# Optimization experiments

Hardware: AMD Instinct MI355X
Metric: run time of the kernel (lower is better)

The kernel has to match this reference:

```python
import jax, jax.numpy as jnp
import numpy as np

N_NODES = 100000
N_EDGES = 1000000
IN_CH = 64
HID = 64
PROJ = 128
N_GRAPHS = 64
BN_EPS = 1e-5


def _glorot(key, shape):
    fan_in, fan_out = shape[0], shape[1]
    lim = (6.0 / (fan_in + fan_out)) ** 0.5
    return jax.random.uniform(key, shape, jnp.float32, -lim, lim)


def setup_inputs() -> dict:
    key = jax.random.key(0)
    ks = jax.random.split(key, 16)
    x = jax.random.normal(ks[0], (N_NODES, IN_CH), jnp.float32)
    edge_index = jax.random.randint(ks[1], (2, N_EDGES), 0, N_NODES, jnp.int64)
    batch = jnp.sort(jax.random.randint(ks[2], (N_NODES,), 0, N_GRAPHS, jnp.int64))
    inp = {
        "x": x, "edge_index": edge_index, "batch": batch,
        # conv1 MLP: Linear(2*in, hid), Linear(hid, hid)
        "c1_w1": _glorot(ks[3], (2 * IN_CH, HID)), "c1_b1": jnp.zeros((HID,), jnp.float32),
        "c1_w2": _glorot(ks[4], (HID, HID)), "c1_b2": jnp.zeros((HID,), jnp.float32),
        "bn1_g": jnp.ones((HID,), jnp.float32), "bn1_b": jnp.zeros((HID,), jnp.float32),
        # conv2 MLP: Linear(2*hid, hid), Linear(hid, hid)
        "c2_w1": _glorot(ks[5], (2 * HID, HID)), "c2_b1": jnp.zeros((HID,), jnp.float32),
        "c2_w2": _glorot(ks[6], (HID, HID)), "c2_b2": jnp.zeros((HID,), jnp.float32),
        "bn2_g": jnp.ones((HID,), jnp.float32), "bn2_b": jnp.zeros((HID,), jnp.float32),
        # projector: Linear(2*hid, proj), BN(proj), Linear(proj, proj)
        "p_w1": _glorot(ks[7], (2 * HID, PROJ)), "p_b1": jnp.zeros((PROJ,), jnp.float32),
        "p_bng": jnp.ones((PROJ,), jnp.float32), "p_bnb": jnp.zeros((PROJ,), jnp.float32),
        "p_w2": _glorot(ks[8], (PROJ, PROJ)), "p_b2": jnp.zeros((PROJ,), jnp.float32),
    }
    return inp


def _edge_conv(x, src, dst, w1, b1, w2, b2):
    # PyG EdgeConv: message = nn(cat([x_i, x_j - x_i])), aggr = max over incoming edges
    xi = x[dst]                                   # [E, C] target features
    xj = x[src]                                   # [E, C] source features
    m = jnp.concatenate([xi, xj - xi], axis=-1)   # [E, 2C]
    h = jax.nn.relu(m @ w1 + b1)
    h = jax.nn.relu(h @ w2 + b2)                  # [E, H]
    out = jax.ops.segment_max(h, dst, num_segments=N_NODES)
    return jnp.where(jnp.isfinite(out), out, 0.0)  # nodes w/o in-edges -> 0


def _batchnorm(x, g, b):
    mu = jnp.mean(x, axis=0)
    var = jnp.mean((x - mu) ** 2, axis=0)  # biased var (training-mode BN)
    return (x - mu) * jax.lax.rsqrt(var + BN_EPS) * g + b


def reference(x, edge_index, batch,
              c1_w1, c1_b1, c1_w2, c1_b2, bn1_g, bn1_b,
              c2_w1, c2_b1, c2_w2, c2_b2, bn2_g, bn2_b,
              p_w1, p_b1, p_bng, p_bnb, p_w2, p_b2):
    src, dst = edge_index[0], edge_index[1]
    h = _edge_conv(x, src, dst, c1_w1, c1_b1, c1_w2, c1_b2)
    h = _batchnorm(h, bn1_g, bn1_b)
    h = _edge_conv(h, src, dst, c2_w1, c2_b1, c2_w2, c2_b2)
    x_node = _batchnorm(h, bn2_g, bn2_b)            # [N, H]
    # graph pooling
    counts = jax.ops.segment_sum(jnp.ones((N_NODES,), x_node.dtype), batch,
                                 num_segments=N_GRAPHS)
    mean_pool = jax.ops.segment_sum(x_node, batch, num_segments=N_GRAPHS) / \
        jnp.maximum(counts, 1.0)[:, None]
    max_pool = jax.ops.segment_max(x_node, batch, num_segments=N_GRAPHS)
    max_pool = jnp.where(jnp.isfinite(max_pool), max_pool, 0.0)
    x_graph = jnp.concatenate([mean_pool, max_pool], axis=1)  # [G, 2H]
    # projector MLP
    z = x_graph @ p_w1 + p_b1
    z = jax.nn.relu(_batchnorm(z, p_bng, p_bnb))
    z_proj = z @ p_w2 + p_b2                        # [G, PROJ]
    return (z_proj, x_node, x_graph)
```

## Files before the change

### kernel.cpp

```cpp
#include <hip/hip_runtime.h>
#include <hip/hip_fp16.h>

constexpr int NN = 100000;
constexpr int NE = 1000000;
constexpr int NG = 64;
constexpr float BN_EPS = 1e-5f;
constexpr int NTILES = NE / 32;
constexpr int NNTILES = NN / 32;
constexpr int NREC = NTILES * 2;

constexpr int NBUK = 196;
constexpr int BINB = 256;
constexpr int BCHUNK = (NE + BINB - 1) / BINB;
constexpr int TABN = NBUK * BINB;

constexpr long H1R_OFF  = 0;
constexpr long XNR_OFF  = 3200000;
constexpr long PART_OFF = 6400000;
constexpr long SC1_OFF  = PART_OFF + 32768;
constexpr long SH1_OFF  = SC1_OFF + 64;
constexpr long SC2_OFF  = SH1_OFF + 64;
constexpr long SH2_OFF  = SC2_OFF + 64;
constexpr long PSUM_OFF = SH2_OFF + 64;
constexpr long PMAX_OFF = PSUM_OFF + 4096;
constexpr long CNT_OFF  = PMAX_OFF + 4096;
constexpr long TAB_OFF  = CNT_OFF + 64;
constexpr long SEDG_OFF = TAB_OFF + 50176;
constexpr long WF1_OFF  = SEDG_OFF + 2000000;
constexpr long WF2_OFF  = WF1_OFF + 6144;
constexpr long RECD_OFF = WF2_OFF + 6144;
constexpr long RECV_OFF = RECD_OFF + 62528;
constexpr long P_OFF    = RECV_OFF + 2000000;
constexpr long Q_OFF    = P_OFF + 3200000;

constexpr long OUT_XNODE = 8192;
constexpr long OUT_XG    = 8192 + 6400000L;

using f16x8 = __attribute__((ext_vector_type(8))) _Float16;
using f32x16 = __attribute__((ext_vector_type(16))) float;

__device__ __forceinline__ unsigned short f2h(float f) {
    return __builtin_bit_cast(unsigned short, (_Float16)f);
}
__device__ __forceinline__ unsigned pkrtz(float a, float b) {
    return __builtin_bit_cast(unsigned, __builtin_amdgcn_cvt_pkrtz(a, b));
}
__device__ __forceinline__ unsigned pk_add_f16(unsigned a, unsigned b) {
    unsigned d;
    asm("v_pk_add_f16 %0, %1, %2" : "=v"(d) : "v"(a), "v"(b));
    return d;
}
__device__ __forceinline__ unsigned pk_max_f16(unsigned a, unsigned b) {
    unsigned d;
    asm("v_pk_max_f16 %0, %1, %2" : "=v"(d) : "v"(a), "v"(b));
    return d;
}
__device__ __forceinline__ float h2f_lo(unsigned u) {
    return (float)__builtin_bit_cast(_Float16, (unsigned short)(u & 0xffffu));
}
__device__ __forceinline__ float h2f_hi(unsigned u) {
    return (float)__builtin_bit_cast(_Float16, (unsigned short)(u >> 16));
}
__device__ __forceinline__ unsigned fenc(float f) {
    unsigned u = __float_as_uint(f);
    return (u & 0x80000000u) ? ~u : (u | 0x80000000u);
}
__device__ __forceinline__ float fdec(unsigned u) {
    return (u & 0x80000000u) ? __uint_as_float(u & 0x7fffffffu) : __uint_as_float(~u);
}
__device__ __forceinline__ int xcd_swz(int bid, int nwg) {
    const int q = nwg >> 3, r = nwg & 7;
    const int x = bid & 7, i = bid >> 3;
    return (x < r ? x * (q + 1) : r * (q + 1) + (x - r) * q) + i;
}

__global__ __launch_bounds__(256) void bin_hist_kernel(
    const int* __restrict__ dst, int* __restrict__ tab)
{
    __shared__ int cnt[NBUK];
    const int t = threadIdx.x, b = blockIdx.x;
    if (t < NBUK) cnt[t] = 0;
    __syncthreads();
    const int lo = b * BCHUNK;
    const int hi = (lo + BCHUNK < NE) ? lo + BCHUNK : NE;
    for (int e = lo + t; e < hi; e += 256) atomicAdd(&cnt[dst[e] >> 9], 1);
    __syncthreads();
    if (t < NBUK) tab[t * BINB + b] = cnt[t];
}

__global__ __launch_bounds__(1024) void scan_tab_kernel(int* __restrict__ tab)
{
    __shared__ int part[1024];
    const int t = threadIdx.x;
    constexpr int VPT = 49;
    int vals[VPT];
    const int base = t * VPT;
    int s = 0;
    #pragma unroll
    for (int i = 0; i < VPT; ++i) {
        const int idx = base + i;
        const int v = (idx < TABN) ? tab[idx] : 0;
        vals[i] = v; s += v;
    }
    part[t] = s;
    __syncthreads();
    for (int off = 1; off < 1024; off <<= 1) {
        const int u = (t >= off) ? part[t - off] : 0;
        __syncthreads();
        part[t] += u;
        __syncthreads();
    }
    int run = (t == 0) ? 0 : part[t - 1];
    #pragma unroll
    for (int i = 0; i < VPT; ++i) {
        const int idx = base + i;
        if (idx < TABN) { const int v = vals[i]; tab[idx] = run; run += v; }
    }
}

__global__ __launch_bounds__(256) void bin_scatter_kernel(
    const int* __restrict__ src, const int* __restrict__ dst,
    const int* __restrict__ tab, int2* __restrict__ ebin)
{
    __shared__ int basec[NBUK];
    __shared__ int cur[NBUK];
    const int t = threadIdx.x, b = blockIdx.x;
    if (t < NBUK) { basec[t] = tab[t * BINB + b]; cur[t] = 0; }
    __syncthreads();
    const int lo = b * BCHUNK;
    const int hi = (lo + BCHUNK < NE) ? lo + BCHUNK : NE;
    for (int e = lo + t; e < hi; e += 256) {
        const int d = dst[e];
        const int k = d >> 9;
        const int pos = basec[k] + atomicAdd(&cur[k], 1);
        ebin[pos] = make_int2(src[e], d);
    }
}

__global__ __launch_bounds__(256) void bucket_sort_kernel(
    const int2* __restrict__ ebin, const int* __restrict__ tab,
    int2* __restrict__ sedge)
{
    __shared__ int hist[512];
    __shared__ int part[256];
    const int t = threadIdx.x, k = blockIdx.x;
    const int start = tab[k * BINB];
    const int end = (k == NBUK - 1) ? NE : tab[(k + 1) * BINB];
    hist[t * 2] = 0; hist[t * 2 + 1] = 0;
    __syncthreads();
    for (int e = start + t; e < end; e += 256) atomicAdd(&hist[ebin[e].y & 511], 1);
    __syncthreads();
    const int v0 = hist[t * 2], v1 = hist[t * 2 + 1];
    part[t] = v0 + v1;
    __syncthreads();
    for (int off = 1; off < 256; off <<= 1) {
        const int u = (t >= off) ? part[t - off] : 0;
        __syncthreads();
        part[t] += u;
        __syncthreads();
    }
    int run = (t == 0) ? 0 : part[t - 1];
    hist[t * 2] = run;
    hist[t * 2 + 1] = run + v0;
    __syncthreads();
    for (int e = start + t; e < end; e += 256) {
        const int2 v = ebin[e];
        const int pos = start + atomicAdd(&hist[v.y & 511], 1);
        sedge[pos] = v;
    }
}

__global__ __launch_bounds__(256) void prep_weights(
    const float* __restrict__ w1, const float* __restrict__ w2,
    unsigned short* __restrict__ wf)
{
    const int idx = blockIdx.x * 256 + threadIdx.x;
    if (idx >= 12288) return;
    const int sec = idx >> 12;
    const int j = idx & 4095;
    const int f = j >> 9, rem = j & 511, ln = rem >> 3, i = rem & 7;
    const int t = f >> 2, ks = f & 3;
    const int k = ks * 16 + (ln >> 5) * 8 + i, c = t * 32 + (ln & 31);
    float v;
    if (sec == 0)      v = w1[k * 64 + c] - w1[(64 + k) * 64 + c];
    else if (sec == 1) v = w1[(64 + k) * 64 + c];
    else               v = w2[k * 64 + c];
    wf[idx] = f2h(v);
}

template<bool NORM>
__global__ __launch_bounds__(256) void nodegemm_kernel(
    const void* __restrict__ xin,
    const unsigned short* __restrict__ wfrag,
    const float* __restrict__ b1,
    const float* __restrict__ scale, const float* __restrict__ shift,
    unsigned short* __restrict__ P, unsigned short* __restrict__ Q)
{
    __shared__ unsigned short wlds[8192];
    {
        const uint4* wsrc = reinterpret_cast<const uint4*>(wfrag);
        uint4* wdst = reinterpret_cast<uint4*>(wlds);
        #pragma unroll
        for (int i = 0; i < 4; ++i) wdst[threadIdx.x + i * 256] = wsrc[threadIdx.x + i * 256];
    }
    __syncthreads();

    const int wid = threadIdx.x >> 6, lane = threadIdx.x & 63;
    const int hi = lane >> 5, ln32 = lane & 31;
    const int tile = blockIdx.x * 4 + wid;
    if (tile >= NNTILES) return;
    const int node = tile * 32 + ln32;

    f32x16 cpa, cpb, cqa, cqb;
    #pragma unroll
    for (int r = 0; r < 16; ++r) {
        const int row = (r & 3) + 8 * (r >> 2) + 4 * hi;
        cpa[r] = b1[row]; cpb[r] = b1[32 + row];
        cqa[r] = 0.f;     cqb[r] = 0.f;
    }

    #pragma unroll
    for (int ks = 0; ks < 4; ++ks) {
        const int off = ks * 16 + hi * 8;
        float4 a, b;
        if constexpr (!NORM) {
            const float* xr = reinterpret_cast<const float*>(xin) + (long)node * 64;
            a = *reinterpret_cast<const float4*>(xr + off);
            b = *reinterpret_cast<const float4*>(xr + off + 4);
        } else {
            const unsigned* xr = reinterpret_cast<const unsigned*>(xin) + (long)node * 32;
            const uint4 u = *reinterpret_cast<const uint4*>(xr + ks * 8 + hi * 4);
            a.x = h2f_lo(u.x); a.y = h2f_hi(u.x); a.z = h2f_lo(u.y); a.w = h2f_hi(u.y);
            b.x = h2f_lo(u.z); b.y = h2f_hi(u.z); b.z = h2f_lo(u.w); b.w = h2f_hi(u.w);
            const float4 s0 = *reinterpret_cast<const float4*>(scale + off);
            const float4 s1 = *reinterpret_cast<const float4*>(scale + off + 4);
            const float4 h0 = *reinterpret_cast<const float4*>(shift + off);
            const float4 h1 = *reinterpret_cast<const float4*>(shift + off + 4);
            a.x = fmaf(a.x, s0.x, h0.x); a.y = fmaf(a.y, s0.y, h0.y);
            a.z = fmaf(a.z, s0.z, h0.z); a.w = fmaf(a.w, s0.w, h0.w);
            b.x = fmaf(b.x, s1.x, h1.x); b.y = fmaf(b.y, s1.y, h1.y);
            b.z = fmaf(b.z, s1.z, h1.z); b.w = fmaf(b.w, s1.w, h1.w);
        }
        uint4 uu;
        uu.x = pkrtz(a.x, a.y); uu.y = pkrtz(a.z, a.w);
        uu.z = pkrtz(b.x, b.y); uu.w = pkrtz(b.z, b.w);
        const f16x8 bfr = __builtin_bit_cast(f16x8, uu);
        const f16x8 ap0 = *reinterpret_cast<const f16x8*>(&wlds[(0 * 4 + ks) * 512 + lane * 8]);
        const f16x8 ap1 = *reinterpret_cast<const f16x8*>(&wlds[(1 * 4 + ks) * 512 + lane * 8]);
        const f16x8 aq0 = *reinterpret_cast<const f16x8*>(&wlds[4096 + (0 * 4 + ks) * 512 + lane * 8]);
        const f16x8 aq1 = *reinterpret_cast<const f16x8*>(&wlds[4096 + (1 * 4 + ks) * 512 + lane * 8]);
        cpa = __builtin_amdgcn_mfma_f32_32x32x16_f16(ap0, bfr, cpa, 0, 0, 0);
        cpb = __builtin_amdgcn_mfma_f32_32x32x16_f16(ap1, bfr, cpb, 0, 0, 0);
        cqa = __builtin_amdgcn_mfma_f32_32x32x16_f16(aq0, bfr, cqa, 0, 0, 0);
        cqb = __builtin_amdgcn_mfma_f32_32x32x16_f16(aq1, bfr, cqb, 0, 0, 0);
    }

    unsigned short* Pr = P + (long)node * 64;
    unsigned short* Qr = Q + (long)node * 64;
    #pragma unroll
    for (int t = 0; t < 2; ++t) {
        const f32x16 cp = t ? cpb : cpa;
        const f32x16 cq = t ? cqb : cqa;
        #pragma unroll
        for (int g2 = 0; g2 < 4; ++g2) {
            uint2 up, uq;
            up.x = pkrtz(cp[4 * g2 + 0], cp[4 * g2 + 1]);
            up.y = pkrtz(cp[4 * g2 + 2], cp[4 * g2 + 3]);
            uq.x = pkrtz(cq[4 * g2 + 0], cq[4 * g2 + 1]);
            uq.y = pkrtz(cq[4 * g2 + 2], cq[4 * g2 + 3]);
            const int co = t * 32 + 8 * g2 + 4 * hi;
            *reinterpret_cast<uint2*>(Pr + co) = up;
            *reinterpret_cast<uint2*>(Qr + co) = uq;
        }
    }
}

__global__ __launch_bounds__(256) void edgeconv_kernel(
    const unsigned short* __restrict__ P, const unsigned short* __restrict__ Q,
    const int2* __restrict__ sedge,
    const unsigned short* __restrict__ w2frag,
    const float* __restrict__ b2,
    unsigned* __restrict__ out,
    int* __restrict__ recd, unsigned* __restrict__ recv)
{
    __shared__ unsigned short wlds[4096];
    {
        const uint4* wsrc = reinterpret_cast<const uint4*>(w2frag);
        uint4* wdst = reinterpret_cast<uint4*>(wlds);
        #pragma unroll
        for (int i = 0; i < 2; ++i) wdst[threadIdx.x + i * 256] = wsrc[threadIdx.x + i * 256];
    }
    __syncthreads();

    const int wid  = threadIdx.x >> 6;
    const int lane = threadIdx.x & 63;
    const int hi   = lane >> 5;
    const int ln32 = lane & 31;
    const int tile = xcd_swz(blockIdx.x, gridDim.x) * 4 + wid;
    if (tile >= NTILES) return;

    const int2 sd = sedge[tile * 32 + ln32];
    const int s = sd.x, d = sd.y;
    const unsigned short* __restrict__ Pr = P + (long)d * 64;
    const unsigned short* __restrict__ Qr = Q + (long)s * 64;

    f32x16 c2a, c2b;
    #pragma unroll
    for (int r = 0; r < 16; ++r) {
        const int row = (r & 3) + 8 * (r >> 2) + 4 * hi;
        c2a[r] = b2[row];
        c2b[r] = b2[32 + row];
    }

    #pragma unroll
    for (int ks = 0; ks < 4; ++ks) {
        const int co = ks * 16 + hi * 8;
        const uint4 pu = *reinterpret_cast<const uint4*>(Pr + co);
        const uint4 qu = *reinterpret_cast<const uint4*>(Qr + co);
        uint4 hh;
        hh.x = pk_max_f16(pk_add_f16(pu.x, qu.x), 0u);
        hh.y = pk_max_f16(pk_add_f16(pu.y, qu.y), 0u);
        hh.z = pk_max_f16(pk_add_f16(pu.z, qu.z), 0u);
        hh.w = pk_max_f16(pk_add_f16(pu.w, qu.w), 0u);
        const f16x8 bfr = __builtin_bit_cast(f16x8, hh);
        const f16x8 a0 = *reinterpret_cast<const f16x8*>(&wlds[(0 * 4 + ks) * 512 + lane * 8]);
        const f16x8 a1 = *reinterpret_cast<const f16x8*>(&wlds[(1 * 4 + ks) * 512 + lane * 8]);
        c2a = __builtin_amdgcn_mfma_f32_32x32x16_f16(a0, bfr, c2a, 0, 0, 0);
        c2b = __builtin_amdgcn_mfma_f32_32x32x16_f16(a1, bfr, c2b, 0, 0, 0);
    }

    unsigned pkc[16];
    #pragma unroll
    for (int q = 0; q < 8; ++q) {
        pkc[q]     = pk_max_f16(pkrtz(c2a[2 * q], c2a[2 * q + 1]), 0u);
        pkc[8 + q] = pk_max_f16(pkrtz(c2b[2 * q], c2b[2 * q + 1]), 0u);
    }

    #pragma unroll
    for (int st = 1; st < 32; st <<= 1) {
        const int dn = __shfl_down(d, st, 32);
        const bool take = (ln32 + st < 32) && (dn == d);
        #pragma unroll
        for (int i = 0; i < 16; ++i) {
            const unsigned o = __shfl_down(pkc[i], st, 32);
            const unsigned m = pk_max_f16(pkc[i], o);
            pkc[i] = take ? m : pkc[i];
        }
    }
    const int dprev = __shfl_up(d, 1, 32);
    const bool leader = (ln32 == 0) || (d != dprev);
    const unsigned lm = (unsigned)(__ballot(leader) & 0xffffffffull);
    const int L31 = 31 - __builtin_clz(lm);

    if (leader) {
        if (ln32 != 0 && ln32 != L31) {
            unsigned* row = out + (long)d * 32;
            #pragma unroll
            for (int g2 = 0; g2 < 4; ++g2) {
                *reinterpret_cast<uint2*>(row + 4 * g2 + 2 * hi) =
                    make_uint2(pkc[2 * g2], pkc[2 * g2 + 1]);
                *reinterpret_cast<uint2*>(row + 16 + 4 * g2 + 2 * hi) =
                    make_uint2(pkc[8 + 2 * g2], pkc[8 + 2 * g2 + 1]);
            }
        }
        if (ln32 == 0) {
            unsigned* row = recv + (long)(tile * 2) * 32;
            #pragma unroll
            for (int g2 = 0; g2 < 4; ++g2) {
                *reinterpret_cast<uint2*>(row + 4 * g2 + 2 * hi) =
                    make_uint2(pkc[2 * g2], pkc[2 * g2 + 1]);
                *reinterpret_cast<uint2*>(row + 16 + 4 * g2 + 2 * hi) =
                    make_uint2(pkc[8 + 2 * g2], pkc[8 + 2 * g2 + 1]);
            }
            if (hi == 0) recd[tile * 2] = d;
        }
        if (ln32 == L31) {
            unsigned* row = recv + (long)(tile * 2 + 1) * 32;
            #pragma unroll
            for (int g2 = 0; g2 < 4; ++g2) {
                *reinterpret_cast<uint2*>(row + 4 * g2 + 2 * hi) =
                    make_uint2(pkc[2 * g2], pkc[2 * g2 + 1]);
                *reinterpret_cast<uint2*>(row + 16 + 4 * g2 + 2 * hi) =
                    make_uint2(pkc[8 + 2 * g2], pkc[8 + 2 * g2 + 1]);
            }
            if (hi == 0) recd[tile * 2 + 1] = d;
        }
    }
}

__global__ __launch_bounds__(256) void fixup_kernel(
    const int* __restrict__ recd, const unsigned* __restrict__ recv,
    unsigned* __restrict__ out)
{
    const int wid = threadIdx.x >> 6;
    const int half = (threadIdx.x >> 5) & 1;
    const int c2 = threadIdx.x & 31;
    const int r = blockIdx.x * 8 + wid * 2 + half;
    if (r >= NREC) return;
    const int d = recd[r];
    int lo = r, hi = r;
    while (lo > 0 && recd[lo - 1] == d) --lo;
    while (hi + 1 < NREC && recd[hi + 1] == d) ++hi;
    unsigned m = 0u;
    for (int rr = lo; rr <= hi; ++rr) m = pk_max_f16(m, recv[(long)rr * 32 + c2]);
    out[(long)d * 32 + c2] = m;
}

__global__ __launch_bounds__(256) void stats_kernel(
    const unsigned* __restrict__ h, float* __restrict__ partial)
{
    __shared__ float red[4][256];
    const int tid = threadIdx.x;
    const int c2 = tid & 31, r = tid >> 5;
    float s0 = 0.f, ss0 = 0.f, s1 = 0.f, ss1 = 0.f;
    for (int v = blockIdx.x * 8 + r; v < NN; v += 256 * 8) {
        const unsigned u = h[(long)v * 32 + c2];
        const float a = h2f_lo(u), b = h2f_hi(u);
        s0 += a; ss0 += a * a; s1 += b; ss1 += b * b;
    }
    red[0][tid] = s0; red[1][tid] = ss0; red[2][tid] = s1; red[3][tid] = ss1;
    __syncthreads();
    if (r == 0) {
        float S0 = 0.f, SS0 = 0.f, S1 = 0.f, SS1 = 0.f;
        #pragma unroll
        for (int q = 0; q < 8; ++q) {
            S0 += red[0][c2 + q * 32]; SS0 += red[1][c2 + q * 32];
            S1 += red[2][c2 + q * 32]; SS1 += red[3][c2 + q * 32];
        }
        partial[blockIdx.x * 128 + 2 * c2]     = S0;
        partial[blockIdx.x * 128 + 2 * c2 + 1] = S1;
        partial[blockIdx.x * 128 + 64 + 2 * c2]     = SS0;
        partial[blockIdx.x * 128 + 64 + 2 * c2 + 1] = SS1;
    }
}

__global__ __launch_bounds__(256) void bn_finalize_kernel(
    const float* __restrict__ partial,
    const float* __restrict__ g, const float* __restrict__ b,
    float* __restrict__ scale, float* __restrict__ shift)
{
    __shared__ float red[2][256];
    const int tid = threadIdx.x;
    const int c = tid & 63, q = tid >> 6;
    float S = 0.f, SS = 0.f;
    for (int bb = q * 64; bb < q * 64 + 64; ++bb) {
        S += partial[bb * 128 + c];
        SS += partial[bb * 128 + 64 + c];
    }
    red[0][tid] = S; red[1][tid] = SS;
    __syncthreads();
    if (q == 0) {
        #pragma unroll
        for (int p = 1; p < 4; ++p) { S += red[0][c + p * 64]; SS += red[1][c + p * 64]; }
        const float invN = 1.0f / (float)NN;
        const float mu = S * invN;
        const float var = SS * invN - mu * mu;
        const float sc = g[c] * rsqrtf(var + BN_EPS);
        scale[c] = sc;
        shift[c] = b[c] - mu * sc;
    }
}

constexpr int NPB = 512;
__global__ __launch_bounds__(256) void nodepass_kernel(
    const unsigned* __restrict__ xnr, float* __restrict__ xn,
    const int* __restrict__ batch,
    const float* __restrict__ scale, const float* __restrict__ shift,
    float* __restrict__ poolsum, unsigned* __restrict__ poolmax, int* __restrict__ counts)
{
    const int base = blockIdx.x * NPB;
    const int r = threadIdx.x >> 5, c2 = threadIdx.x & 31;
    const float sc0 = scale[2 * c2], sc1 = scale[2 * c2 + 1];
    const float sh0 = shift[2 * c2], sh1 = shift[2 * c2 + 1];
    int curg = -1; float rs0 = 0.f, rs1 = 0.f, rm0 = -INFINITY, rm1 = -INFINITY; int rc = 0;
    const int vend = (base + NPB < NN) ? base + NPB : NN;
    for (int v = base + r; v < vend; v += 8) {
        const unsigned u = xnr[(long)v * 32 + c2];
        const float v0 = fmaf(h2f_lo(u), sc0, sh0);
        const float v1 = fmaf(h2f_hi(u), sc1, sh1);
        *reinterpret_cast<float2*>(xn + (long)v * 64 + 2 * c2) = make_float2(v0, v1);
        const int g = batch[v];
        if (g != curg) {
            if (curg >= 0) {
                atomicAdd(poolsum + curg * 64 + 2 * c2, rs0);
                atomicAdd(poolsum + curg * 64 + 2 * c2 + 1, rs1);
                atomicMax(poolmax + curg * 64 + 2 * c2, fenc(rm0));
                atomicMax(poolmax + curg * 64 + 2 * c2 + 1, fenc(rm1));
                if (c2 == 0) atomicAdd(counts + curg, rc);
            }
            curg = g; rs0 = rs1 = 0.f; rm0 = rm1 = -INFINITY; rc = 0;
        }
        rs0 += v0; rs1 += v1; rm0 = fmaxf(rm0, v0); rm1 = fmaxf(rm1, v1); ++rc;
    }
    if (curg >= 0) {
        atomicAdd(poolsum + curg * 64 + 2 * c2, rs0);
        atomicAdd(poolsum + curg * 64 + 2 * c2 + 1, rs1);
        atomicMax(poolmax + curg * 64 + 2 * c2, fenc(rm0));
        atomicMax(poolmax + curg * 64 + 2 * c2 + 1, fenc(rm1));
        if (c2 == 0) atomicAdd(counts + curg, rc);
    }
}

__global__ __launch_bounds__(512) void final_kernel(
    const float* __restrict__ poolsum, const unsigned* __restrict__ poolmax,
    const int* __restrict__ counts,
    const float* __restrict__ p_w1, const float* __restrict__ p_b1,
    const float* __restrict__ p_bng, const float* __restrict__ p_bnb,
    const float* __restrict__ p_w2, const float* __restrict__ p_b2,
    float* __restrict__ out)
{
    __shared__ float xg[64][128];
    __shared__ float znl[64 * 129];
    __shared__ float red[2][512];
    __shared__ float scsh[2][128];
    const int tid = threadIdx.x;

    #pragma unroll
    for (int i = 0; i < 16; ++i) {
        const int e2 = tid + i * 512;
        const int g = e2 >> 7, col = e2 & 127;
        float val;
        if (col < 64) {
            const float cnt = fmaxf((float)counts[g], 1.f);
            val = poolsum[g * 64 + col] / cnt;
        } else {
            const unsigned u = poolmax[g * 64 + col - 64];
            val = (u == 0u) ? 0.f : fdec(u);
        }
        xg[g][col] = val;
        out[OUT_XG + e2] = val;
    }
    __syncthreads();

    const int gg = tid >> 7, t = tid & 127;
    float z[16];
    #pragma unroll
    for (int gi = 0; gi < 16; ++gi) z[gi] = p_b1[t];
    for (int j = 0; j < 128; ++j) {
        const float wv = p_w1[j * 128 + t];
        #pragma unroll
        for (int gi = 0; gi < 16; ++gi) z[gi] = fmaf(xg[gg * 16 + gi][j], wv, z[gi]);
    }

    float s = 0.f, ss = 0.f;
    #pragma unroll
    for (int gi = 0; gi < 16; ++gi) { s += z[gi]; ss += z[gi] * z[gi]; }
    red[0][tid] = s; red[1][tid] = ss;
    __syncthreads();
    if (gg == 0) {
        float S = 0.f, SS = 0.f;
        #pragma unroll
        for (int q = 0; q < 4; ++q) { S += red[0][t + q * 128]; SS += red[1][t + q * 128]; }
        const float mu = S / 64.f;
        const float var = SS / 64.f - mu * mu;
        const float sc = p_bng[t] * rsqrtf(var + BN_EPS);
        scsh[0][t] = sc;
        scsh[1][t] = p_bnb[t] - mu * sc;
    }
    __syncthreads();
    const float sc = scsh[0][t], sh = scsh[1][t];
    #pragma unroll
    for (int gi = 0; gi < 16; ++gi) {
        const float zn = fmaxf(fmaf(z[gi], sc, sh), 0.f);
        znl[(gg * 16 + gi) * 129 + t] = zn;
    }
    __syncthreads();

    float zp[16];
    #pragma unroll
    for (int gi = 0; gi < 16; ++gi) zp[gi] = p_b2[t];
    for (int c = 0; c < 128; ++c) {
        const float wv = p_w2[c * 128 + t];
        #pragma unroll
        for (int gi = 0; gi < 16; ++gi) zp[gi] = fmaf(znl[(gg * 16 + gi) * 129 + c], wv, zp[gi]);
    }
    #pragma unroll
    for (int gi = 0; gi < 16; ++gi) out[(gg * 16 + gi) * 128 + t] = zp[gi];
}

extern "C" void kernel_launch(void* const* d_in, const int* in_sizes, int n_in,
                              void* d_out, int out_size, void* d_ws, size_t ws_size,
                              hipStream_t stream)
{
    const float* x     = (const float*)d_in[0];
    const int*   eidx  = (const int*)d_in[1];
    const int*   batch = (const int*)d_in[2];
    const float* c1w1  = (const float*)d_in[3];
    const float* c1b1  = (const float*)d_in[4];
    const float* c1w2  = (const float*)d_in[5];
    const float* c1b2  = (const float*)d_in[6];
    const float* bn1g  = (const float*)d_in[7];
    const float* bn1b  = (const float*)d_in[8];
    const float* c2w1  = (const float*)d_in[9];
    const float* c2b1  = (const float*)d_in[10];
    const float* c2w2  = (const float*)d_in[11];
    const float* c2b2  = (const float*)d_in[12];
    const float* bn2g  = (const float*)d_in[13];
    const float* bn2b  = (const float*)d_in[14];
    const float* pw1   = (const float*)d_in[15];
    const float* pb1   = (const float*)d_in[16];
    const float* pbng  = (const float*)d_in[17];
    const float* pbnb  = (const float*)d_in[18];
    const float* pw2   = (const float*)d_in[19];
    const float* pb2   = (const float*)d_in[20];

    const int* src = eidx;
    const int* dst = eidx + NE;

    float* ws  = (float*)d_ws;
    float* o   = (float*)d_out;
    unsigned* h1r = (unsigned*)(ws + H1R_OFF);
    unsigned* xnr = (unsigned*)(ws + XNR_OFF);
    float* xnode = o + OUT_XNODE;
    int* tab   = (int*)(ws + TAB_OFF);
    int2* ebin  = (int2*)(ws + H1R_OFF);
    int2* sedge = (int2*)(ws + SEDG_OFF);
    unsigned short* wf1 = (unsigned short*)(ws + WF1_OFF);
    unsigned short* wf2 = (unsigned short*)(ws + WF2_OFF);
    int* recd  = (int*)(ws + RECD_OFF);
    unsigned* recv = (unsigned*)(ws + RECV_OFF);
    unsigned short* Pb = (unsigned short*)(ws + P_OFF);
    unsigned short* Qb = (unsigned short*)(ws + Q_OFF);

    prep_weights<<<48, 256, 0, stream>>>(c1w1, c1w2, wf1);
    prep_weights<<<48, 256, 0, stream>>>(c2w1, c2w2, wf2);

    bin_hist_kernel<<<BINB, 256, 0, stream>>>(dst, tab);
    scan_tab_kernel<<<1, 1024, 0, stream>>>(tab);
    bin_scatter_kernel<<<BINB, 256, 0, stream>>>(src, dst, tab, ebin);
    bucket_sort_kernel<<<NBUK, 256, 0, stream>>>(ebin, tab, sedge);

    hipMemsetAsync(h1r, 0, (size_t)NN * 64 * 2, stream);
    hipMemsetAsync(xnr, 0, (size_t)NN * 64 * 2, stream);
    hipMemsetAsync(ws + PSUM_OFF, 0, (4096 + 4096 + 64) * 4, stream);

    const int ngGrid   = (NNTILES + 3) / 4;
    const int convGrid = (NTILES + 3) / 4;
    const int fixGrid  = (NREC + 7) / 8;

    nodegemm_kernel<false><<<ngGrid, 256, 0, stream>>>(
        x, wf1, c1b1, nullptr, nullptr, Pb, Qb);
    edgeconv_kernel<<<convGrid, 256, 0, stream>>>(
        Pb, Qb, sedge, wf1 + 8192, c1b2, h1r, recd, recv);
    fixup_kernel<<<fixGrid, 256, 0, stream>>>(recd, recv, h1r);
    stats_kernel<<<256, 256, 0, stream>>>(h1r, ws + PART_OFF);
    bn_finalize_kernel<<<1, 256, 0, stream>>>(ws + PART_OFF, bn1g, bn1b,
                                              ws + SC1_OFF, ws + SH1_OFF);
    nodegemm_kernel<true><<<ngGrid, 256, 0, stream>>>(
        h1r, wf2, c2b1, ws + SC1_OFF, ws + SH1_OFF, Pb, Qb);
    edgeconv_kernel<<<convGrid, 256, 0, stream>>>(
        Pb, Qb, sedge, wf2 + 8192, c2b2, xnr, recd, recv);
    fixup_kernel<<<fixGrid, 256, 0, stream>>>(recd, recv, xnr);
    stats_kernel<<<256, 256, 0, stream>>>(xnr, ws + PART_OFF);
    bn_finalize_kernel<<<1, 256, 0, stream>>>(ws + PART_OFF, bn2g, bn2b,
                                              ws + SC2_OFF, ws + SH2_OFF);
    nodepass_kernel<<<(NN + NPB - 1) / NPB, 256, 0, stream>>>(
        xnr, xnode, batch, ws + SC2_OFF, ws + SH2_OFF,
        ws + PSUM_OFF, (unsigned*)(ws + PMAX_OFF), (int*)(ws + CNT_OFF));
    final_kernel<<<1, 512, 0, stream>>>(
        ws + PSUM_OFF, (unsigned*)(ws + PMAX_OFF), (int*)(ws + CNT_OFF),
        pw1, pb1, pbng, pbnb, pw2, pb2, o);
}
```

Before: 356.0 us.

## Cut kernel launches via last-block ticket fusion and merge small setup kernels

The table scan is folded into the histogram kernel and the BN finalize into the stats kernel, using an atomic ticket so the last block finishes the work. The two weight-prep launches become one, and the two memsets become one contiguous memset. Separately, edgeconv now issues all P/Q gathers before the MFMA loop, nodepass uses fewer nodes per block, and final_kernel runs with 1024 threads. The aim is fewer launches and serial single-block kernels, at the cost of threadfence/ticket synchronization and a serial scan done by 256 threads in the last block.

```diff
diff --git a/kernel.cpp b/kernel.cpp
--- a/kernel.cpp
+++ b/kernel.cpp
@@ -24,7 +24,8 @@
 constexpr long PSUM_OFF = SH2_OFF + 64;
 constexpr long PMAX_OFF = PSUM_OFF + 4096;
 constexpr long CNT_OFF  = PMAX_OFF + 4096;
-constexpr long TAB_OFF  = CNT_OFF + 64;
+constexpr long TICK_OFF = CNT_OFF + 64;
+constexpr long TAB_OFF  = TICK_OFF + 16;
 constexpr long SEDG_OFF = TAB_OFF + 50176;
 constexpr long WF1_OFF  = SEDG_OFF + 2000000;
 constexpr long WF2_OFF  = WF1_OFF + 6144;
@@ -75,9 +76,11 @@
 }
 
 __global__ __launch_bounds__(256) void bin_hist_kernel(
-    const int* __restrict__ dst, int* __restrict__ tab)
+    const int* __restrict__ dst, int* __restrict__ tab, int* __restrict__ ticket)
 {
     __shared__ int cnt[NBUK];
+    __shared__ int part[256];
+    __shared__ int flag;
     const int t = threadIdx.x, b = blockIdx.x;
     if (t < NBUK) cnt[t] = 0;
     __syncthreads();
@@ -86,35 +89,30 @@
     for (int e = lo + t; e < hi; e += 256) atomicAdd(&cnt[dst[e] >> 9], 1);
     __syncthreads();
     if (t < NBUK) tab[t * BINB + b] = cnt[t];
-}
-
-__global__ __launch_bounds__(1024) void scan_tab_kernel(int* __restrict__ tab)
-{
-    __shared__ int part[1024];
-    const int t = threadIdx.x;
-    constexpr int VPT = 49;
-    int vals[VPT];
-    const int base = t * VPT;
+    __syncthreads();
+    if (t == 0) {
+        __threadfence();
+        flag = (atomicAdd(ticket, 1) == BINB - 1) ? 1 : 0;
+    }
+    __syncthreads();
+    if (!flag) return;
+    __threadfence();
+    constexpr int STRIP = TABN / 256;
     int s = 0;
-    #pragma unroll
-    for (int i = 0; i < VPT; ++i) {
-        const int idx = base + i;
-        const int v = (idx < TABN) ? tab[idx] : 0;
-        vals[i] = v; s += v;
-    }
+    for (int i = 0; i < STRIP; ++i) s += tab[t * STRIP + i];
     part[t] = s;
     __syncthreads();
-    for (int off = 1; off < 1024; off <<= 1) {
+    for (int off = 1; off < 256; off <<= 1) {
         const int u = (t >= off) ? part[t - off] : 0;
         __syncthreads();
         part[t] += u;
         __syncthreads();
     }
     int run = (t == 0) ? 0 : part[t - 1];
-    #pragma unroll
-    for (int i = 0; i < VPT; ++i) {
-        const int idx = base + i;
-        if (idx < TABN) { const int v = vals[i]; tab[idx] = run; run += v; }
+    for (int i = 0; i < STRIP; ++i) {
+        const int v = tab[t * STRIP + i];
+        tab[t * STRIP + i] = run;
+        run += v;
     }
 }
 
@@ -171,11 +169,16 @@
 }
 
 __global__ __launch_bounds__(256) void prep_weights(
-    const float* __restrict__ w1, const float* __restrict__ w2,
+    const float* __restrict__ c1w1, const float* __restrict__ c1w2,
+    const float* __restrict__ c2w1, const float* __restrict__ c2w2,
     unsigned short* __restrict__ wf)
 {
-    const int idx = blockIdx.x * 256 + threadIdx.x;
-    if (idx >= 12288) return;
+    const int gidx = blockIdx.x * 256 + threadIdx.x;
+    if (gidx >= 24576) return;
+    const bool second = gidx >= 12288;
+    const int idx = second ? gidx - 12288 : gidx;
+    const float* __restrict__ w1 = second ? c2w1 : c1w1;
+    const float* __restrict__ w2 = second ? c2w2 : c1w2;
     const int sec = idx >> 12;
     const int j = idx & 4095;
     const int f = j >> 9, rem = j & 511, ln = rem >> 3, i = rem & 7;
@@ -185,7 +188,7 @@
     if (sec == 0)      v = w1[k * 64 + c] - w1[(64 + k) * 64 + c];
     else if (sec == 1) v = w1[(64 + k) * 64 + c];
     else               v = w2[k * 64 + c];
-    wf[idx] = f2h(v);
+    wf[gidx] = f2h(v);
 }
 
 template<bool NORM>
@@ -304,6 +307,14 @@
     const unsigned short* __restrict__ Pr = P + (long)d * 64;
     const unsigned short* __restrict__ Qr = Q + (long)s * 64;
 
+    uint4 pu[4], qu[4];
+    #pragma unroll
+    for (int ks = 0; ks < 4; ++ks) {
+        const int co = ks * 16 + hi * 8;
+        pu[ks] = *reinterpret_cast<const uint4*>(Pr + co);
+        qu[ks] = *reinterpret_cast<const uint4*>(Qr + co);
+    }
+
     f32x16 c2a, c2b;
     #pragma unroll
     for (int r = 0; r < 16; ++r) {
@@ -314,14 +325,11 @@
 
     #pragma unroll
     for (int ks = 0; ks < 4; ++ks) {
-        const int co = ks * 16 + hi * 8;
-        const uint4 pu = *reinterpret_cast<const uint4*>(Pr + co);
-        const uint4 qu = *reinterpret_cast<const uint4*>(Qr + co);
         uint4 hh;
-        hh.x = pk_max_f16(pk_add_f16(pu.x, qu.x), 0u);
-        hh.y = pk_max_f16(pk_add_f16(pu.y, qu.y), 0u);
-        hh.z = pk_max_f16(pk_add_f16(pu.z, qu.z), 0u);
-        hh.w = pk_max_f16(pk_add_f16(pu.w, qu.w), 0u);
+        hh.x = pk_max_f16(pk_add_f16(pu[ks].x, qu[ks].x), 0u);
+        hh.y = pk_max_f16(pk_add_f16(pu[ks].y, qu[ks].y), 0u);
+        hh.z = pk_max_f16(pk_add_f16(pu[ks].z, qu[ks].z), 0u);
+        hh.w = pk_max_f16(pk_add_f16(pu[ks].w, qu[ks].w), 0u);
         const f16x8 bfr = __builtin_bit_cast(f16x8, hh);
         const f16x8 a0 = *reinterpret_cast<const f16x8*>(&wlds[(0 * 4 + ks) * 512 + lane * 8]);
         const f16x8 a1 = *reinterpret_cast<const f16x8*>(&wlds[(1 * 4 + ks) * 512 + lane * 8]);
@@ -407,16 +415,20 @@
 }
 
 __global__ __launch_bounds__(256) void stats_kernel(
-    const unsigned* __restrict__ h, float* __restrict__ partial)
+    const unsigned* __restrict__ h, float* __restrict__ partial,
+    const float* __restrict__ g, const float* __restrict__ b,
+    float* __restrict__ scale, float* __restrict__ shift, int* __restrict__ ticket)
 {
     __shared__ float red[4][256];
+    __shared__ float red2[2][256];
+    __shared__ int flag;
     const int tid = threadIdx.x;
     const int c2 = tid & 31, r = tid >> 5;
     float s0 = 0.f, ss0 = 0.f, s1 = 0.f, ss1 = 0.f;
     for (int v = blockIdx.x * 8 + r; v < NN; v += 256 * 8) {
         const unsigned u = h[(long)v * 32 + c2];
-        const float a = h2f_lo(u), b = h2f_hi(u);
-        s0 += a; ss0 += a * a; s1 += b; ss1 += b * b;
+        const float a = h2f_lo(u), bb = h2f_hi(u);
+        s0 += a; ss0 += a * a; s1 += bb; ss1 += bb * bb;
     }
     red[0][tid] = s0; red[1][tid] = ss0; red[2][tid] = s1; red[3][tid] = ss1;
     __syncthreads();
@@ -432,26 +444,25 @@
         partial[blockIdx.x * 128 + 64 + 2 * c2]     = SS0;
         partial[blockIdx.x * 128 + 64 + 2 * c2 + 1] = SS1;
     }
-}
-
-__global__ __launch_bounds__(256) void bn_finalize_kernel(
-    const float* __restrict__ partial,
-    const float* __restrict__ g, const float* __restrict__ b,
-    float* __restrict__ scale, float* __restrict__ shift)
-{
-    __shared__ float red[2][256];
-    const int tid = threadIdx.x;
+    __syncthreads();
+    if (tid == 0) {
+        __threadfence();
+        flag = (atomicAdd(ticket, 1) == 255) ? 1 : 0;
+    }
+    __syncthreads();
+    if (!flag) return;
+    __threadfence();
     const int c = tid & 63, q = tid >> 6;
     float S = 0.f, SS = 0.f;
-    for (int bb = q * 64; bb < q * 64 + 64; ++bb) {
-        S += partial[bb * 128 + c];
-        SS += partial[bb * 128 + 64 + c];
-    }
-    red[0][tid] = S; red[1][tid] = SS;
+    for (int bb2 = q * 64; bb2 < q * 64 + 64; ++bb2) {
+        S += partial[bb2 * 128 + c];
+        SS += partial[bb2 * 128 + 64 + c];
+    }
+    red2[0][tid] = S; red2[1][tid] = SS;
     __syncthreads();
     if (q == 0) {
         #pragma unroll
-        for (int p = 1; p < 4; ++p) { S += red[0][c + p * 64]; SS += red[1][c + p * 64]; }
+        for (int p = 1; p < 4; ++p) { S += red2[0][c + p * 64]; SS += red2[1][c + p * 64]; }
         const float invN = 1.0f / (float)NN;
         const float mu = S * invN;
         const float var = SS * invN - mu * mu;
@@ -461,7 +472,7 @@
     }
 }
 
-constexpr int NPB = 512;
+constexpr int NPB = 256;
 __global__ __launch_bounds__(256) void nodepass_kernel(
     const unsigned* __restrict__ xnr, float* __restrict__ xn,
     const int* __restrict__ batch,
@@ -501,7 +512,7 @@
     }
 }
 
-__global__ __launch_bounds__(512) void final_kernel(
+__global__ __launch_bounds__(1024) void final_kernel(
     const float* __restrict__ poolsum, const unsigned* __restrict__ poolmax,
     const int* __restrict__ counts,
     const float* __restrict__ p_w1, const float* __restrict__ p_b1,
@@ -511,13 +522,13 @@
 {
     __shared__ float xg[64][128];
     __shared__ float znl[64 * 129];
-    __shared__ float red[2][512];
+    __shared__ float red[2][1024];
     __shared__ float scsh[2][128];
     const int tid = threadIdx.x;
 
     #pragma unroll
-    for (int i = 0; i < 16; ++i) {
-        const int e2 = tid + i * 512;
+    for (int i = 0; i < 8; ++i) {
+        const int e2 = tid + i * 1024;
         const int g = e2 >> 7, col = e2 & 127;
         float val;
         if (col < 64) {
@@ -533,24 +544,24 @@
     __syncthreads();
 
     const int gg = tid >> 7, t = tid & 127;
-    float z[16];
-    #pragma unroll
-    for (int gi = 0; gi < 16; ++gi) z[gi] = p_b1[t];
+    float z[8];
+    #pragma unroll
+    for (int gi = 0; gi < 8; ++gi) z[gi] = p_b1[t];
     for (int j = 0; j < 128; ++j) {
         const float wv = p_w1[j * 128 + t];
         #pragma unroll
-        for (int gi = 0; gi < 16; ++gi) z[gi] = fmaf(xg[gg * 16 + gi][j], wv, z[gi]);
+        for (int gi = 0; gi < 8; ++gi) z[gi] = fmaf(xg[gg * 8 + gi][j], wv, z[gi]);
     }
 
     float s = 0.f, ss = 0.f;
     #pragma unroll
-    for (int gi = 0; gi < 16; ++gi) { s += z[gi]; ss += z[gi] * z[gi]; }
+    for (int gi = 0; gi < 8; ++gi) { s += z[gi]; ss += z[gi] * z[gi]; }
     red[0][tid] = s; red[1][tid] = ss;
     __syncthreads();
     if (gg == 0) {
         float S = 0.f, SS = 0.f;
         #pragma unroll
-        for (int q = 0; q < 4; ++q) { S += red[0][t + q * 128]; SS += red[1][t + q * 128]; }
+        for (int q = 0; q < 8; ++q) { S += red[0][t + q * 128]; SS += red[1][t + q * 128]; }
         const float mu = S / 64.f;
         const float var = SS / 64.f - mu * mu;
         const float sc = p_bng[t] * rsqrtf(var + BN_EPS);
@@ -560,22 +571,22 @@
     __syncthreads();
     const float sc = scsh[0][t], sh = scsh[1][t];
     #pragma unroll
-    for (int gi = 0; gi < 16; ++gi) {
+    for (int gi = 0; gi < 8; ++gi) {
         const float zn = fmaxf(fmaf(z[gi], sc, sh), 0.f);
-        znl[(gg * 16 + gi) * 129 + t] = zn;
-    }
-    __syncthreads();
-
-    float zp[16];
-    #pragma unroll
-    for (int gi = 0; gi < 16; ++gi) zp[gi] = p_b2[t];
+        znl[(gg * 8 + gi) * 129 + t] = zn;
+    }
+    __syncthreads();
+
+    float zp[8];
+    #pragma unroll
+    for (int gi = 0; gi < 8; ++gi) zp[gi] = p_b2[t];
     for (int c = 0; c < 128; ++c) {
         const float wv = p_w2[c * 128 + t];
         #pragma unroll
-        for (int gi = 0; gi < 16; ++gi) zp[gi] = fmaf(znl[(gg * 16 + gi) * 129 + c], wv, zp[gi]);
-    }
-    #pragma unroll
-    for (int gi = 0; gi < 16; ++gi) out[(gg * 16 + gi) * 128 + t] = zp[gi];
+        for (int gi = 0; gi < 8; ++gi) zp[gi] = fmaf(znl[(gg * 8 + gi) * 129 + c], wv, zp[gi]);
+    }
+    #pragma unroll
+    for (int gi = 0; gi < 8; ++gi) out[(gg * 8 + gi) * 128 + t] = zp[gi];
 }
 
 extern "C" void kernel_launch(void* const* d_in, const int* in_sizes, int n_in,
@@ -612,6 +623,7 @@
     unsigned* h1r = (unsigned*)(ws + H1R_OFF);
     unsigned* xnr = (unsigned*)(ws + XNR_OFF);
     float* xnode = o + OUT_XNODE;
+    int* tick  = (int*)(ws + TICK_OFF);
     int* tab   = (int*)(ws + TAB_OFF);
     int2* ebin  = (int2*)(ws + H1R_OFF);
     int2* sedge = (int2*)(ws + SEDG_OFF);
@@ -622,17 +634,15 @@
     unsigned short* Pb = (unsigned short*)(ws + P_OFF);
     unsigned short* Qb = (unsigned short*)(ws + Q_OFF);
 
-    prep_weights<<<48, 256, 0, stream>>>(c1w1, c1w2, wf1);
-    prep_weights<<<48, 256, 0, stream>>>(c2w1, c2w2, wf2);
-
-    bin_hist_kernel<<<BINB, 256, 0, stream>>>(dst, tab);
-    scan_tab_kernel<<<1, 1024, 0, stream>>>(tab);
+    hipMemsetAsync(ws + PSUM_OFF, 0, (4096 + 4096 + 64 + 16) * 4, stream);
+
+    prep_weights<<<96, 256, 0, stream>>>(c1w1, c1w2, c2w1, c2w2, wf1);
+
+    bin_hist_kernel<<<BINB, 256, 0, stream>>>(dst, tab, tick + 0);
     bin_scatter_kernel<<<BINB, 256, 0, stream>>>(src, dst, tab, ebin);
     bucket_sort_kernel<<<NBUK, 256, 0, stream>>>(ebin, tab, sedge);
 
-    hipMemsetAsync(h1r, 0, (size_t)NN * 64 * 2, stream);
-    hipMemsetAsync(xnr, 0, (size_t)NN * 64 * 2, stream);
-    hipMemsetAsync(ws + PSUM_OFF, 0, (4096 + 4096 + 64) * 4, stream);
+    hipMemsetAsync(h1r, 0, (size_t)NN * 64 * 2 * 2, stream);
 
     const int ngGrid   = (NNTILES + 3) / 4;
     const int convGrid = (NTILES + 3) / 4;
@@ -643,21 +653,19 @@
     edgeconv_kernel<<<convGrid, 256, 0, stream>>>(
         Pb, Qb, sedge, wf1 + 8192, c1b2, h1r, recd, recv);
     fixup_kernel<<<fixGrid, 256, 0, stream>>>(recd, recv, h1r);
-    stats_kernel<<<256, 256, 0, stream>>>(h1r, ws + PART_OFF);
-    bn_finalize_kernel<<<1, 256, 0, stream>>>(ws + PART_OFF, bn1g, bn1b,
-                                              ws + SC1_OFF, ws + SH1_OFF);
+    stats_kernel<<<256, 256, 0, stream>>>(h1r, ws + PART_OFF, bn1g, bn1b,
+                                          ws + SC1_OFF, ws + SH1_OFF, tick + 1);
     nodegemm_kernel<true><<<ngGrid, 256, 0, stream>>>(
         h1r, wf2, c2b1, ws + SC1_OFF, ws + SH1_OFF, Pb, Qb);
     edgeconv_kernel<<<convGrid, 256, 0, stream>>>(
         Pb, Qb, sedge, wf2 + 8192, c2b2, xnr, recd, recv);
     fixup_kernel<<<fixGrid, 256, 0, stream>>>(recd, recv, xnr);
-    stats_kernel<<<256, 256, 0, stream>>>(xnr, ws + PART_OFF);
-    bn_finalize_kernel<<<1, 256, 0, stream>>>(ws + PART_OFF, bn2g, bn2b,
-                                              ws + SC2_OFF, ws + SH2_OFF);
+    stats_kernel<<<256, 256, 0, stream>>>(xnr, ws + PART_OFF, bn2g, bn2b,
+                                          ws + SC2_OFF, ws + SH2_OFF, tick + 2);
     nodepass_kernel<<<(NN + NPB - 1) / NPB, 256, 0, stream>>>(
         xnr, xnode, batch, ws + SC2_OFF, ws + SH2_OFF,
         ws + PSUM_OFF, (unsigned*)(ws + PMAX_OFF), (int*)(ws + CNT_OFF));
-    final_kernel<<<1, 512, 0, stream>>>(
+    final_kernel<<<1, 1024, 0, stream>>>(
         ws + PSUM_OFF, (unsigned*)(ws + PMAX_OFF), (int*)(ws + CNT_OFF),
         pw1, pb1, pbng, pbnb, pw2, pb2, o);
 }
```

Measured after the change: 373.6 us. 1.05x slower.
